# Kernel tuning notes

Measured on AMD Instinct MI355X. Metric: run time of the kernel, lower is better.

The kernel has to match this reference:

```python
import jax, jax.numpy as jnp
import numpy as np

# ---- grid / frustum config (from default grid_config & data_config) ----
DB = (1.0, 60.0, 1.0)                 # dbound
OGH, OGW, DS = 256, 704, 16           # input size, downsample
FH, FW = OGH // DS, OGW // DS         # 16, 44
DEPTH = int(round((DB[1] - DB[0]) / DB[2]))  # 59 depth bins
NX0, NX1, NZ = 128, 128, 1            # BEV grid
DX = np.array([0.8, 0.8, 20.0], np.float32)
BX = np.array([-51.2 + 0.4, -51.2 + 0.4, 0.0], np.float32)  # row0 + dx/2


def _frustum():
    # (D, FH, FW, 3): pixel (u, v, depth)
    ds = jnp.broadcast_to(jnp.arange(DB[0], DB[1], DB[2], dtype=jnp.float32).reshape(-1, 1, 1), (DEPTH, FH, FW))
    xs = jnp.broadcast_to(jnp.linspace(0.0, OGW - 1.0, FW, dtype=jnp.float32).reshape(1, 1, FW), (DEPTH, FH, FW))
    ys = jnp.broadcast_to(jnp.linspace(0.0, OGH - 1.0, FH, dtype=jnp.float32).reshape(1, FH, 1), (DEPTH, FH, FW))
    return jnp.stack([xs, ys, ds], axis=-1)


def _geometry(rots, trans, intrins, post_rots, post_trans, bda):
    # pixel frustum -> ego-frame 3D points; (B, N, D, FH, FW, 3)
    pts = _frustum() - post_trans[:, :, None, None, None, :]
    pts = jnp.einsum('bnij,bndhwj->bndhwi', jnp.linalg.inv(post_rots), pts)
    pts = jnp.concatenate([pts[..., :2] * pts[..., 2:3], pts[..., 2:3]], axis=-1)
    comb = jnp.einsum('bnij,bnjk->bnik', rots, jnp.linalg.inv(intrins))
    pts = jnp.einsum('bnij,bndhwj->bndhwi', comb, pts) + trans[:, :, None, None, None, :]
    pts = jnp.einsum('bij,bndhwj->bndhwi', bda, pts)
    return pts


def _voxel_pool(geom, vol):
    # geom: (B,N,D,FH,FW,3), vol: (B,N,D,FH,FW,C) -> BEV (B, C*NZ, NX0, NX1)
    B, C = vol.shape[0], vol.shape[-1]
    gidx = jnp.floor((geom - (BX - DX / 2.0)) / DX).astype(jnp.int32)
    kept = ((gidx[..., 0] >= 0) & (gidx[..., 0] < NX0)
            & (gidx[..., 1] >= 0) & (gidx[..., 1] < NX1)
            & (gidx[..., 2] >= 0) & (gidx[..., 2] < NZ))
    bidx = jnp.broadcast_to(jnp.arange(B, dtype=jnp.int32).reshape(B, 1, 1, 1, 1), gidx.shape[:-1])
    flat = ((bidx * NZ + gidx[..., 2]) * NX0 + gidx[..., 0]) * NX1 + gidx[..., 1]
    nvox = B * NZ * NX0 * NX1
    flat = jnp.where(kept, flat, nvox).reshape(-1)      # dump bucket for culled pts
    feats = vol.reshape(-1, C)
    bev = jax.ops.segment_sum(feats, flat, num_segments=nvox + 1)[:nvox]
    bev = bev.reshape(B, NZ, NX0, NX1, C)
    bev = jnp.moveaxis(bev, -1, 2).reshape(B, NZ * C, NX0, NX1)  # z-major channel cat
    return bev


def setup_inputs() -> dict:
    key = jax.random.key(0)
    B, N, CIN, CT = 4, 6, 512, 64
    k1, k2 = jax.random.split(key, 2)
    x = jax.random.normal(k1, (B, N, CIN, FH, FW), dtype=jnp.float32)
    weight = jax.random.normal(k2, (DEPTH + CT, CIN), dtype=jnp.float32) * 0.02
    bias = jnp.zeros((DEPTH + CT,), dtype=jnp.float32)
    # cam->ego rotation (cam z forward -> ego x, cam x right -> ego -y, cam y down -> ego -z)
    Rcam = jnp.asarray(np.array([[0., 0., 1.], [-1., 0., 0.], [0., -1., 0.]], np.float32))
    rots = jnp.tile(Rcam, (B, N, 1, 1))
    trans = jnp.zeros((B, N, 3), dtype=jnp.float32)
    K = jnp.asarray(np.array([[600., 0., 352.], [0., 600., 128.], [0., 0., 1.]], np.float32))
    intrins = jnp.tile(K, (B, N, 1, 1))
    post_rots = jnp.tile(jnp.eye(3, dtype=jnp.float32), (B, N, 1, 1))
    post_trans = jnp.zeros((B, N, 3), dtype=jnp.float32)
    bda = jnp.tile(jnp.eye(3, dtype=jnp.float32), (B, 1, 1))
    return dict(x=x, rots=rots, trans=trans, intrins=intrins, post_rots=post_rots,
                post_trans=post_trans, bda=bda, weight=weight, bias=bias)


def reference(x, rots, trans, intrins, post_rots, post_trans, bda, weight, bias):
    # 1x1 depth/context head (eval mode): (B,N,Cin,H,W) -> (B,N,D+C,H,W)
    out = jnp.einsum('bnchw,oc->bnohw', x, weight) + bias[None, None, :, None, None]
    depth = jax.nn.softmax(out[:, :, :DEPTH], axis=2)      # (B,N,D,H,W)
    feat = out[:, :, DEPTH:]                               # (B,N,C,H,W)
    # depth-context outer product -> frustum volume (B,N,D,H,W,C)
    vol = jnp.einsum('bndhw,bnchw->bndhwc', depth, feat)
    geom = _geometry(rots, trans, intrins, post_rots, post_trans, bda)
    bev = _voxel_pool(geom, vol)                           # (B, C*NZ, 128, 128)
    return bev, depth
```

## Files before the change

kernel.cpp:

```cpp
#include <hip/hip_runtime.h>
#include <math.h>

#define CIN   512
#define NOUT  123
#define DEPN  59
#define CT    64
#define B_    4
#define N_    6
#define FH    16
#define FW    44
#define HW    704
#define NPIX  (B_*N_*HW)
#define NX    128
#define BEV_ELEMS (B_*CT*NX*NX)
#define DEPTH_OFF BEV_ELEMS

#define WS_WB   1920
#define WS_PS   (WS_WB + 32768)
#define WS_FS   (WS_PS + NPIX*64)
#define WS_C    (WS_FS + NPIX*64)
#define WS_VOX  (WS_C + B_*FW*DEPN*64)
#define WS_MIXF (WS_VOX + B_*FW*DEPN)

typedef short bf16x8 __attribute__((ext_vector_type(8)));
typedef float f32x4  __attribute__((ext_vector_type(4)));

__device__ inline unsigned short f2bf(float f) {
    unsigned u = __float_as_uint(f);
    return (unsigned short)((u + 0x7fffu + ((u >> 16) & 1u)) >> 16);
}

__device__ inline void inv3d(const double* m, double* o) {
    #pragma clang fp contract(off)
    double c00 = m[4]*m[8] - m[5]*m[7];
    double c01 = m[5]*m[6] - m[3]*m[8];
    double c02 = m[3]*m[7] - m[4]*m[6];
    double det = m[0]*c00 + m[1]*c01 + m[2]*c02;
    o[0] = c00/det; o[1] = (m[2]*m[7]-m[1]*m[8])/det; o[2] = (m[1]*m[5]-m[2]*m[4])/det;
    o[3] = c01/det; o[4] = (m[0]*m[8]-m[2]*m[6])/det; o[5] = (m[2]*m[3]-m[0]*m[5])/det;
    o[6] = c02/det; o[7] = (m[1]*m[6]-m[0]*m[7])/det; o[8] = (m[0]*m[4]-m[1]*m[3])/det;
}
__device__ inline void mm3d(const double* a, const double* b, double* o) {
    #pragma clang fp contract(off)
    for (int i = 0; i < 3; ++i)
        for (int k = 0; k < 3; ++k)
            o[i*3+k] = (a[i*3+0]*b[0*3+k] + a[i*3+1]*b[1*3+k]) + a[i*3+2]*b[2*3+k];
}

#define K1A   4608
#define K1T   13824
__global__ __launch_bounds__(256, 2) void k1_gemm(const float* __restrict__ x,
                                                  const float* __restrict__ W,
                                                  const float* __restrict__ bias,
                                                  float* __restrict__ ws,
                                                  float* __restrict__ dout) {
    __shared__ __align__(16) unsigned short s16[2 * K1T];
    const int tid = threadIdx.x;
    const int wave = tid >> 6, lane = tid & 63;
    const int l15 = lane & 15, quad = lane >> 4;
    const int bn = blockIdx.y;
    const int pixbase = blockIdx.x * 64;
    const float* xg = x + (size_t)bn * CIN * HW + pixbase;
    const int cpack = tid >> 4;
    const int pix4 = (tid & 15) * 4;
    const int wo  = tid >> 3;
    const int wsub = tid & 7;

    f32x4 acc[8] = {};
    float4 xr0, xr1, xr2, xr3;
    float4 wf[8];
    const float4 zf4 = {0.f, 0.f, 0.f, 0.f};
    {
        const float* src = xg + (size_t)(4 * cpack) * HW + pix4;
        xr0 = *(const float4*)(src);
        xr1 = *(const float4*)(src + HW);
        xr2 = *(const float4*)(src + 2 * HW);
        xr3 = *(const float4*)(src + 3 * HW);
        #pragma unroll
        for (int i = 0; i < 4; ++i) {
            const int o = wo + 32 * i;
            if (o < NOUT) {
                const float* wp = W + (size_t)o * CIN + wsub * 8;
                wf[2 * i]     = *(const float4*)(wp);
                wf[2 * i + 1] = *(const float4*)(wp + 4);
            } else { wf[2 * i] = zf4; wf[2 * i + 1] = zf4; }
        }
    }
    #pragma unroll
    for (int it = 0; it < 8; ++it) {
        const int buf = it & 1;
        unsigned short* sa = s16 + buf * K1T;
        unsigned short* sb = sa + K1A;
        {
            const float* f0 = (const float*)&xr0; const float* f1 = (const float*)&xr1;
            const float* f2 = (const float*)&xr2; const float* f3 = (const float*)&xr3;
            #pragma unroll
            for (int i = 0; i < 4; ++i) {
                uint2 pk;
                pk.x = (unsigned)f2bf(f0[i]) | ((unsigned)f2bf(f1[i]) << 16);
                pk.y = (unsigned)f2bf(f2[i]) | ((unsigned)f2bf(f3[i]) << 16);
                *(uint2*)&sa[(pix4 + i) * 72 + 4 * cpack] = pk;
            }
            #pragma unroll
            for (int i = 0; i < 4; ++i) {
                const float* fw = (const float*)&wf[2 * i];
                uint4 pk;
                pk.x = (unsigned)f2bf(fw[0]) | ((unsigned)f2bf(fw[1]) << 16);
                pk.y = (unsigned)f2bf(fw[2]) | ((unsigned)f2bf(fw[3]) << 16);
                pk.z = (unsigned)f2bf(fw[4]) | ((unsigned)f2bf(fw[5]) << 16);
                pk.w = (unsigned)f2bf(fw[6]) | ((unsigned)f2bf(fw[7]) << 16);
                *(uint4*)&sb[(wo + 32 * i) * 72 + wsub * 8] = pk;
            }
        }
        if (it < 7) {
            const int ck = (it + 1) * 64;
            const float* src = xg + (size_t)(ck + 4 * cpack) * HW + pix4;
            xr0 = *(const float4*)(src);
            xr1 = *(const float4*)(src + HW);
            xr2 = *(const float4*)(src + 2 * HW);
            xr3 = *(const float4*)(src + 3 * HW);
            #pragma unroll
            for (int i = 0; i < 4; ++i) {
                const int o = wo + 32 * i;
                if (o < NOUT) {
                    const float* wp = W + (size_t)o * CIN + ck + wsub * 8;
                    wf[2 * i]     = *(const float4*)(wp);
                    wf[2 * i + 1] = *(const float4*)(wp + 4);
                } else { wf[2 * i] = zf4; wf[2 * i + 1] = zf4; }
            }
        }
        __syncthreads();
        #pragma unroll
        for (int ks = 0; ks < 64; ks += 32) {
            const bf16x8 a = *(const bf16x8*)&sa[(wave * 16 + l15) * 72 + ks + quad * 8];
            #pragma unroll
            for (int nt = 0; nt < 8; ++nt) {
                const bf16x8 b = *(const bf16x8*)&sb[(nt * 16 + l15) * 72 + ks + quad * 8];
                acc[nt] = __builtin_amdgcn_mfma_f32_16x16x32_bf16(a, b, acc[nt], 0, 0, 0);
            }
        }
    }
    float* sred = (float*)s16;
    const int b = bn / N_, n = bn - b * N_;
    {
        float bb[8];
        #pragma unroll
        for (int nt = 0; nt < 8; ++nt) {
            int o = nt * 16 + l15;
            bb[nt] = (o < NOUT) ? bias[o] : 0.0f;
        }
        float* ps = ws + WS_PS;
        float* fs = ws + WS_FS;
        #pragma unroll
        for (int reg = 0; reg < 4; ++reg) {
            int pixl = wave * 16 + quad * 4 + reg;
            int pix = pixbase + pixl;
            int h = pix / FW, w = pix - h * FW;
            size_t row = (size_t)(b * FW + w) * 96 + n * FH + h;
            float v[4]; float m = -INFINITY;
            #pragma unroll
            for (int nt = 0; nt < 4; ++nt) {
                v[nt] = acc[nt][reg] + bb[nt];
                if (nt * 16 + l15 < DEPN) m = fmaxf(m, v[nt]);
            }
            #pragma unroll
            for (int msk = 8; msk >= 1; msk >>= 1) m = fmaxf(m, __shfl_xor(m, msk, 64));
            float e[4], s = 0.0f;
            #pragma unroll
            for (int nt = 0; nt < 4; ++nt) {
                e[nt] = (nt * 16 + l15 < DEPN) ? expf(v[nt] - m) : 0.0f;
                s += e[nt];
            }
            #pragma unroll
            for (int msk = 8; msk >= 1; msk >>= 1) s += __shfl_xor(s, msk, 64);
            const float inv = 1.0f / s;
            #pragma unroll
            for (int nt = 0; nt < 4; ++nt) {
                int o = nt * 16 + l15;
                if (o < DEPN) {
                    float p = e[nt] * inv;
                    ps[row * 64 + o] = p;
                    sred[pixl * 65 + o] = p;
                } else fs[row * 64 + (o - DEPN)] = v[nt];
            }
            #pragma unroll
            for (int nt = 4; nt < 8; ++nt) {
                int o = nt * 16 + l15;
                if (o < NOUT) fs[row * 64 + (o - DEPN)] = acc[nt][reg] + bb[nt];
            }
        }
    }
    __syncthreads();
    for (int o = wave; o < DEPN; o += 4)
        dout[DEPTH_OFF + ((size_t)bn * DEPN + o) * HW + pixbase + lane] = sred[lane * 65 + o];
    {
        const int gbid = bn * 11 + blockIdx.x;
        float4 z = {0.f, 0.f, 0.f, 0.f};
        for (int i = gbid * 256 + tid; i < BEV_ELEMS / 4; i += 264 * 256)
            *(float4*)(dout + 4 * (size_t)i) = z;
        if (gbid == 0 && tid == 0) ((int*)(ws + WS_MIXF))[0] = 0;
    }
}

#define DQ2 16
__global__ __launch_bounds__(256) void k2b_geom(
        const float* __restrict__ rots,  const float* __restrict__ trans,
        const float* __restrict__ intr,  const float* __restrict__ prots,
        const float* __restrict__ ptrans,const float* __restrict__ bda,
        float* __restrict__ ws,          float* __restrict__ dout) {
    __shared__ float sF[96][64];
    __shared__ float sP[DQ2][100];
    __shared__ unsigned short sv16[DQ2 * 96];
    __shared__ __align__(16) double sG[96 * 9];
    __shared__ double sTd[N_][33];
    __shared__ int sflag[DQ2];
    const int tid = threadIdx.x;
    const int bw = blockIdx.x;
    const int b = bw / FW, w = bw - b * FW;
    const int dbase = blockIdx.y * DQ2;
    const int nd = min(DQ2, DEPN - dbase);

    {
        const float* fsrc = ws + WS_FS + (size_t)bw * (96 * 64);
        const float* psrc = ws + WS_PS + (size_t)bw * (96 * 64);
        for (int i = tid; i < 96 * 16; i += 256) {
            int j = i >> 4, c4 = (i & 15) * 4;
            *(float4*)&sF[j][c4] = *(const float4*)(fsrc + j * 64 + c4);
        }
        for (int i = tid; i < 96 * 4; i += 256) {
            int j = i >> 2, q = i & 3;
            const float4 p4 = *(const float4*)(psrc + j * 64 + dbase + 4 * q);
            sP[4 * q + 0][j] = p4.x; sP[4 * q + 1][j] = p4.y;
            sP[4 * q + 2][j] = p4.z; sP[4 * q + 3][j] = p4.w;
        }
    }
    if (tid < N_) {
        #pragma clang fp contract(off)
        int t = b * N_ + tid;
        double* X = sTd[tid];
        double PR[9], Kd[9], Rd[9], Bd[9];
        for (int i = 0; i < 9; ++i) PR[i] = (double)prots[t * 9 + i];
        for (int i = 0; i < 9; ++i) Kd[i] = (double)intr[t * 9 + i];
        for (int i = 0; i < 9; ++i) Rd[i] = (double)rots[t * 9 + i];
        for (int i = 0; i < 9; ++i) Bd[i] = (double)bda[b * 9 + i];
        double iPR[9]; inv3d(PR, iPR);
        for (int i = 0; i < 9; ++i) X[i] = iPR[i];
        for (int i = 0; i < 3; ++i) X[9 + i] = (double)ptrans[t * 3 + i];
        double iK[9];  inv3d(Kd, iK);
        double comb[9]; mm3d(Rd, iK, comb);
        for (int i = 0; i < 9; ++i) X[12 + i] = comb[i];
        for (int i = 0; i < 3; ++i) X[21 + i] = (double)trans[t * 3 + i];
        for (int i = 0; i < 9; ++i) X[24 + i] = Bd[i];
    }
    __syncthreads();
    if (tid < 96) {
        #pragma clang fp contract(off)
        int j = tid, n = j >> 4, h = j & 15;
        const double* T = sTd[n];
        const double xs = (w == 43) ? 703.0 : (double)w * (703.0 / 43.0);
        const double ys = (double)(h * 17);
        const double u0 = xs - T[9];
        const double u1 = ys - T[10];
        double pA[3], pB[3];
        #pragma unroll
        for (int k = 0; k < 3; ++k) {
            pA[k] = (T[3*k]*u0 + T[3*k+1]*u1) - T[3*k+2]*T[11];
            pB[k] = T[3*k+2];
        }
        double q0c[3] = { pA[0]*pA[2], pA[0]*pB[2] + pB[0]*pA[2], pB[0]*pB[2] };
        double q1c[3] = { pA[1]*pA[2], pA[1]*pB[2] + pB[1]*pA[2], pB[1]*pB[2] };
        double q2c[3] = { pA[2], pB[2], 0.0 };
        double rc[3][3], gc[3][3];
        #pragma unroll
        for (int r = 0; r < 3; ++r)
            #pragma unroll
            for (int k = 0; k < 3; ++k)
                rc[r][k] = ((T[12+3*r]*q0c[k] + T[13+3*r]*q1c[k]) + T[14+3*r]*q2c[k])
                           + ((k == 0) ? T[21+r] : 0.0);
        #pragma unroll
        for (int g = 0; g < 3; ++g)
            #pragma unroll
            for (int k = 0; k < 3; ++k)
                gc[g][k] = (T[24+3*g]*rc[0][k] + T[25+3*g]*rc[1][k]) + T[26+3*g]*rc[2][k];
        #pragma unroll
        for (int q = 0; q < 9; ++q) sG[j * 9 + q] = gc[q / 3][q % 3];
    }
    __syncthreads();

    {
        const double BXY = (double)(-51.2000007629394531f);
        for (int idx = tid; idx < nd * 96; idx += 256) {
            int dl = idx / 96, j = idx - dl * 96;
            const double* G = &sG[j * 9];
            const double dsv = (double)(dbase + dl + 1);
            const double g0 = (G[2] * dsv + G[1]) * dsv + G[0];
            const double g1 = (G[5] * dsv + G[4]) * dsv + G[3];
            const double g2 = (G[8] * dsv + G[7]) * dsv + G[6];
            const double fx = floor((g0 - BXY) * 1.25);
            const double fy = floor((g1 - BXY) * 1.25);
            const bool keep = (fx >= 0.0) & (fx < 128.0) & (fy >= 0.0) & (fy < 128.0) &
                              (g2 >= -10.0) & (g2 < 10.0);
            sv16[idx] = keep ? (unsigned short)((int)fx * NX + (int)fy)
                             : (unsigned short)0xFFFF;
        }
    }
    __syncthreads();

    {
        const int dl = tid >> 4, s = tid & 15;
        int u = -1, mix = 0;
        const int base = dl * 96 + s * 6;
        #pragma unroll
        for (int t = 0; t < 6; ++t) {
            int v = sv16[base + t];
            if (v != 0xFFFF) { if (u < 0) u = v; else if (v != u) mix = 1; }
        }
        #pragma unroll
        for (int msk = 1; msk < 16; msk <<= 1) {
            int uo = __shfl_xor(u, msk, 64);
            int mo = __shfl_xor(mix, msk, 64);
            mix = mix | mo | ((u >= 0 && uo >= 0 && uo != u) ? 1 : 0);
            u = (u < 0) ? uo : u;
        }
        if (s == 0 && dl < nd) sflag[dl] = mix ? -2 : u;
    }
    for (int idx = tid; idx < nd * 96; idx += 256) {
        if (sv16[idx] == 0xFFFF) {
            int dl = idx / 96, j = idx - dl * 96;
            sP[dl][j] = 0.0f;
        }
    }
    __syncthreads();

    const int dl = tid >> 4, ci = tid & 15;
    if (dl < nd) {
        const int flag = sflag[dl];
        if (ci == 0)
            ((int*)(ws + WS_VOX))[bw * DEPN + dbase + dl] = (flag >= 0) ? flag : -1;
        if (flag >= 0) {
            float ax = 0.f, ay = 0.f, az = 0.f, aw = 0.f;
            for (int jj = 0; jj < 96; jj += 4) {
                const float4 pv = *(const float4*)&sP[dl][jj];
                const float4 f0 = *(const float4*)&sF[jj + 0][4 * ci];
                const float4 f1 = *(const float4*)&sF[jj + 1][4 * ci];
                const float4 f2 = *(const float4*)&sF[jj + 2][4 * ci];
                const float4 f3 = *(const float4*)&sF[jj + 3][4 * ci];
                ax = fmaf(pv.x, f0.x, ax); ay = fmaf(pv.x, f0.y, ay);
                az = fmaf(pv.x, f0.z, az); aw = fmaf(pv.x, f0.w, aw);
                ax = fmaf(pv.y, f1.x, ax); ay = fmaf(pv.y, f1.y, ay);
                az = fmaf(pv.y, f1.z, az); aw = fmaf(pv.y, f1.w, aw);
                ax = fmaf(pv.z, f2.x, ax); ay = fmaf(pv.z, f2.y, ay);
                az = fmaf(pv.z, f2.z, az); aw = fmaf(pv.z, f2.w, aw);
                ax = fmaf(pv.w, f3.x, ax); ay = fmaf(pv.w, f3.y, ay);
                az = fmaf(pv.w, f3.z, az); aw = fmaf(pv.w, f3.w, aw);
            }
            float4 st = { ax, ay, az, aw };
            *(float4*)&ws[WS_C + ((size_t)(bw * DEPN + dbase + dl)) * 64 + 4 * ci] = st;
        }
    }
    for (int d2 = 0; d2 < nd; ++d2) {
        if (sflag[d2] == -2) {
            if (tid == 0) atomicOr((int*)(ws + WS_MIXF), 1);
            int c = tid & 63, g = tid >> 6;
            for (int jj = 0; jj < 24; ++jj) {
                int j = g * 24 + jj;
                int v = sv16[d2 * 96 + j];
                if (v != 0xFFFF)
                    atomicAdd(dout + (((size_t)(b * CT + c)) << 14) + v,
                              sP[d2][j] * sF[j][c]);
            }
        }
    }
}

#define CHUNK 128
__global__ __launch_bounds__(256) void k2c_scatter(const float* __restrict__ ws,
                                                   float* __restrict__ dout) {
    __shared__ float acc[64][CHUNK + 4];
    __shared__ int   sVox[FW * DEPN];
    __shared__ short sMatch[FW * DEPN];
    __shared__ int   nMatch;
    const int tid = threadIdx.x;
    const int base = blockIdx.x * CHUNK;
    const int b = blockIdx.y;
    for (int i = tid; i < 64 * (CHUNK + 4); i += 256) (&acc[0][0])[i] = 0.0f;
    if (tid == 0) nMatch = 0;
    const int* vsrc = (const int*)(ws + WS_VOX) + b * (FW * DEPN);
    for (int i = tid; i < FW * DEPN; i += 256) sVox[i] = vsrc[i];
    __syncthreads();
    for (int i = tid; i < FW * DEPN; i += 256) {
        int v = sVox[i];
        if ((unsigned)(v - base) < CHUNK) {
            int m = atomicAdd(&nMatch, 1);
            sMatch[m] = (short)i;
        }
    }
    __syncthreads();
    const int c = tid & 63, quarter = tid >> 6;
    const int nm = nMatch;
    for (int m = quarter; m < nm; m += 4) {
        int e = sMatch[m];
        int lv = sVox[e] - base;
        float val = ws[WS_C + ((size_t)b * (FW * DEPN) + e) * 64 + c];
        atomicAdd(&acc[c][lv], val);
    }
    __syncthreads();
    const int mixed = ((const int*)(ws + WS_MIXF))[0];
    const int wave = tid >> 6, lane = tid & 63;
    float* outb = dout + (((size_t)(b * CT)) << 14) + base;
    if (!mixed) {
        for (int r = wave; r < 64; r += 4) {
            float2 v = { acc[r][lane * 2], acc[r][lane * 2 + 1] };
            *(float2*)(outb + ((size_t)r << 14) + lane * 2) = v;
        }
    } else {
        for (int r = wave; r < 64; r += 4) {
            float2* dst = (float2*)(outb + ((size_t)r << 14) + lane * 2);
            float2 v = *dst;
            v.x += acc[r][lane * 2];
            v.y += acc[r][lane * 2 + 1];
            *dst = v;
        }
    }
}

extern "C" void kernel_launch(void* const* d_in, const int* in_sizes, int n_in,
                              void* d_out, int out_size, void* d_ws, size_t ws_size,
                              hipStream_t stream) {
    const float* x      = (const float*)d_in[0];
    const float* rots   = (const float*)d_in[1];
    const float* trans  = (const float*)d_in[2];
    const float* intr   = (const float*)d_in[3];
    const float* prots  = (const float*)d_in[4];
    const float* ptrans = (const float*)d_in[5];
    const float* bda    = (const float*)d_in[6];
    const float* W      = (const float*)d_in[7];
    const float* bias   = (const float*)d_in[8];
    float* out = (float*)d_out;
    float* ws  = (float*)d_ws;

    k1_gemm<<<dim3(HW / 64, B_ * N_), 256, 0, stream>>>(x, W, bias, ws, out);
    k2b_geom<<<dim3(B_ * FW, 4), 256, 0, stream>>>(rots, trans, intr, prots, ptrans,
                                                   bda, ws, out);
    k2c_scatter<<<dim3(NX * NX / CHUNK, B_), 256, 0, stream>>>(ws, out);
}
```

Baseline: 137.5 us.

## Split GEMM output channels across blocks and replace BEV zero-fill with overflow buffer

The 1x1 conv GEMM now splits its 128 output columns across two blocks per pixel tile, which doubles the grid and halves per-block accumulators and LDS. The first half handles softmax and depth, the second writes context features. The full BEV zero-fill in k1 and the global atomicAdd into the output for mixed-voxel rows are removed. Those contributions are instead appended to a workspace overflow list, which k2c_scatter folds into its shared accumulators before writing each chunk. This makes the final store a plain overwrite, at the cost of x being loaded twice and every scatter block scanning the overflow list.

```diff
diff --git a/kernel.cpp b/kernel.cpp
--- a/kernel.cpp
+++ b/kernel.cpp
@@ -20,7 +20,10 @@
 #define WS_FS   (WS_PS + NPIX*64)
 #define WS_C    (WS_FS + NPIX*64)
 #define WS_VOX  (WS_C + B_*FW*DEPN*64)
-#define WS_MIXF (WS_VOX + B_*FW*DEPN)
+#define WS_OVN  (WS_VOX + B_*FW*DEPN)
+#define WS_OVK  (WS_OVN + 8)
+#define WS_OVD  (WS_OVK + 16384)
+#define OVCAP   16384
 
 typedef short bf16x8 __attribute__((ext_vector_type(8)));
 typedef float f32x4  __attribute__((ext_vector_type(4)));
@@ -48,27 +51,30 @@
 }
 
 #define K1A   4608
-#define K1T   13824
-__global__ __launch_bounds__(256, 2) void k1_gemm(const float* __restrict__ x,
-                                                  const float* __restrict__ W,
-                                                  const float* __restrict__ bias,
-                                                  float* __restrict__ ws,
-                                                  float* __restrict__ dout) {
+#define K1T   9216
+__global__ __launch_bounds__(256) void k1_gemm(const float* __restrict__ x,
+                                               const float* __restrict__ W,
+                                               const float* __restrict__ bias,
+                                               float* __restrict__ ws,
+                                               float* __restrict__ dout) {
     __shared__ __align__(16) unsigned short s16[2 * K1T];
     const int tid = threadIdx.x;
     const int wave = tid >> 6, lane = tid & 63;
     const int l15 = lane & 15, quad = lane >> 4;
     const int bn = blockIdx.y;
-    const int pixbase = blockIdx.x * 64;
+    const int px = blockIdx.x >> 1;
+    const int oh = blockIdx.x & 1;
+    const int pixbase = px * 64;
+    const int o0 = oh * 64;
     const float* xg = x + (size_t)bn * CIN * HW + pixbase;
     const int cpack = tid >> 4;
     const int pix4 = (tid & 15) * 4;
     const int wo  = tid >> 3;
     const int wsub = tid & 7;
 
-    f32x4 acc[8] = {};
+    f32x4 acc[4] = {};
     float4 xr0, xr1, xr2, xr3;
-    float4 wf[8];
+    float4 wf[4];
     const float4 zf4 = {0.f, 0.f, 0.f, 0.f};
     {
         const float* src = xg + (size_t)(4 * cpack) * HW + pix4;
@@ -77,8 +83,8 @@
         xr2 = *(const float4*)(src + 2 * HW);
         xr3 = *(const float4*)(src + 3 * HW);
         #pragma unroll
-        for (int i = 0; i < 4; ++i) {
-            const int o = wo + 32 * i;
+        for (int i = 0; i < 2; ++i) {
+            const int o = o0 + wo + 32 * i;
             if (o < NOUT) {
                 const float* wp = W + (size_t)o * CIN + wsub * 8;
                 wf[2 * i]     = *(const float4*)(wp);
@@ -102,7 +108,7 @@
                 *(uint2*)&sa[(pix4 + i) * 72 + 4 * cpack] = pk;
             }
             #pragma unroll
-            for (int i = 0; i < 4; ++i) {
+            for (int i = 0; i < 2; ++i) {
                 const float* fw = (const float*)&wf[2 * i];
                 uint4 pk;
                 pk.x = (unsigned)f2bf(fw[0]) | ((unsigned)f2bf(fw[1]) << 16);
@@ -120,8 +126,8 @@
             xr2 = *(const float4*)(src + 2 * HW);
             xr3 = *(const float4*)(src + 3 * HW);
             #pragma unroll
-            for (int i = 0; i < 4; ++i) {
-                const int o = wo + 32 * i;
+            for (int i = 0; i < 2; ++i) {
+                const int o = o0 + wo + 32 * i;
                 if (o < NOUT) {
                     const float* wp = W + (size_t)o * CIN + ck + wsub * 8;
                     wf[2 * i]     = *(const float4*)(wp);
@@ -134,7 +140,7 @@
         for (int ks = 0; ks < 64; ks += 32) {
             const bf16x8 a = *(const bf16x8*)&sa[(wave * 16 + l15) * 72 + ks + quad * 8];
             #pragma unroll
-            for (int nt = 0; nt < 8; ++nt) {
+            for (int nt = 0; nt < 4; ++nt) {
                 const bf16x8 b = *(const bf16x8*)&sb[(nt * 16 + l15) * 72 + ks + quad * 8];
                 acc[nt] = __builtin_amdgcn_mfma_f32_16x16x32_bf16(a, b, acc[nt], 0, 0, 0);
             }
@@ -143,10 +149,10 @@
     float* sred = (float*)s16;
     const int b = bn / N_, n = bn - b * N_;
     {
-        float bb[8];
-        #pragma unroll
-        for (int nt = 0; nt < 8; ++nt) {
-            int o = nt * 16 + l15;
+        float bb[4];
+        #pragma unroll
+        for (int nt = 0; nt < 4; ++nt) {
+            int o = o0 + nt * 16 + l15;
             bb[nt] = (o < NOUT) ? bias[o] : 0.0f;
         }
         float* ps = ws + WS_PS;
@@ -157,49 +163,50 @@
             int pix = pixbase + pixl;
             int h = pix / FW, w = pix - h * FW;
             size_t row = (size_t)(b * FW + w) * 96 + n * FH + h;
-            float v[4]; float m = -INFINITY;
-            #pragma unroll
-            for (int nt = 0; nt < 4; ++nt) {
-                v[nt] = acc[nt][reg] + bb[nt];
-                if (nt * 16 + l15 < DEPN) m = fmaxf(m, v[nt]);
-            }
-            #pragma unroll
-            for (int msk = 8; msk >= 1; msk >>= 1) m = fmaxf(m, __shfl_xor(m, msk, 64));
-            float e[4], s = 0.0f;
-            #pragma unroll
-            for (int nt = 0; nt < 4; ++nt) {
-                e[nt] = (nt * 16 + l15 < DEPN) ? expf(v[nt] - m) : 0.0f;
-                s += e[nt];
-            }
-            #pragma unroll
-            for (int msk = 8; msk >= 1; msk >>= 1) s += __shfl_xor(s, msk, 64);
-            const float inv = 1.0f / s;
-            #pragma unroll
-            for (int nt = 0; nt < 4; ++nt) {
-                int o = nt * 16 + l15;
-                if (o < DEPN) {
-                    float p = e[nt] * inv;
-                    ps[row * 64 + o] = p;
-                    sred[pixl * 65 + o] = p;
-                } else fs[row * 64 + (o - DEPN)] = v[nt];
-            }
-            #pragma unroll
-            for (int nt = 4; nt < 8; ++nt) {
-                int o = nt * 16 + l15;
-                if (o < NOUT) fs[row * 64 + (o - DEPN)] = acc[nt][reg] + bb[nt];
-            }
-        }
-    }
-    __syncthreads();
-    for (int o = wave; o < DEPN; o += 4)
-        dout[DEPTH_OFF + ((size_t)bn * DEPN + o) * HW + pixbase + lane] = sred[lane * 65 + o];
-    {
-        const int gbid = bn * 11 + blockIdx.x;
-        float4 z = {0.f, 0.f, 0.f, 0.f};
-        for (int i = gbid * 256 + tid; i < BEV_ELEMS / 4; i += 264 * 256)
-            *(float4*)(dout + 4 * (size_t)i) = z;
-        if (gbid == 0 && tid == 0) ((int*)(ws + WS_MIXF))[0] = 0;
-    }
+            if (oh == 0) {
+                float v[4]; float m = -INFINITY;
+                #pragma unroll
+                for (int nt = 0; nt < 4; ++nt) {
+                    v[nt] = acc[nt][reg] + bb[nt];
+                    if (nt * 16 + l15 < DEPN) m = fmaxf(m, v[nt]);
+                }
+                #pragma unroll
+                for (int msk = 8; msk >= 1; msk >>= 1) m = fmaxf(m, __shfl_xor(m, msk, 64));
+                float e[4], s = 0.0f;
+                #pragma unroll
+                for (int nt = 0; nt < 4; ++nt) {
+                    e[nt] = (nt * 16 + l15 < DEPN) ? expf(v[nt] - m) : 0.0f;
+                    s += e[nt];
+                }
+                #pragma unroll
+                for (int msk = 8; msk >= 1; msk >>= 1) s += __shfl_xor(s, msk, 64);
+                const float inv = 1.0f / s;
+                #pragma unroll
+                for (int nt = 0; nt < 4; ++nt) {
+                    int o = nt * 16 + l15;
+                    if (o < DEPN) {
+                        float p = e[nt] * inv;
+                        ps[row * 64 + o] = p;
+                        sred[pixl * 65 + o] = p;
+                    } else fs[row * 64 + (o - DEPN)] = v[nt];
+                }
+            } else {
+                #pragma unroll
+                for (int nt = 0; nt < 4; ++nt) {
+                    int o = o0 + nt * 16 + l15;
+                    if (o < NOUT) fs[row * 64 + (o - DEPN)] = acc[nt][reg] + bb[nt];
+                }
+            }
+        }
+    }
+    __syncthreads();
+    if (oh == 0) {
+        for (int o = wave; o < DEPN; o += 4)
+            dout[DEPTH_OFF + ((size_t)bn * DEPN + o) * HW + pixbase + lane] =
+                sred[lane * 65 + o];
+    }
+    if (blockIdx.x == 0 && blockIdx.y == 0 && tid == 0)
+        ((int*)(ws + WS_OVN))[0] = 0;
 }
 
 #define DQ2 16
@@ -207,7 +214,7 @@
         const float* __restrict__ rots,  const float* __restrict__ trans,
         const float* __restrict__ intr,  const float* __restrict__ prots,
         const float* __restrict__ ptrans,const float* __restrict__ bda,
-        float* __restrict__ ws,          float* __restrict__ dout) {
+        float* __restrict__ ws) {
     __shared__ float sF[96][64];
     __shared__ float sP[DQ2][100];
     __shared__ unsigned short sv16[DQ2 * 96];
@@ -360,14 +367,19 @@
     }
     for (int d2 = 0; d2 < nd; ++d2) {
         if (sflag[d2] == -2) {
-            if (tid == 0) atomicOr((int*)(ws + WS_MIXF), 1);
             int c = tid & 63, g = tid >> 6;
             for (int jj = 0; jj < 24; ++jj) {
                 int j = g * 24 + jj;
                 int v = sv16[d2 * 96 + j];
-                if (v != 0xFFFF)
-                    atomicAdd(dout + (((size_t)(b * CT + c)) << 14) + v,
-                              sP[d2][j] * sF[j][c]);
+                if (v != 0xFFFF) {
+                    int slot = 0;
+                    if (c == 0) slot = atomicAdd((int*)(ws + WS_OVN), 1);
+                    slot = __shfl(slot, 0, 64);
+                    if (slot < OVCAP) {
+                        if (c == 0) ((int*)(ws + WS_OVK))[slot] = (b << 14) | v;
+                        ws[WS_OVD + (size_t)slot * 64 + c] = sP[d2][j] * sF[j][c];
+                    }
+                }
             }
         }
     }
@@ -404,23 +416,22 @@
         float val = ws[WS_C + ((size_t)b * (FW * DEPN) + e) * 64 + c];
         atomicAdd(&acc[c][lv], val);
     }
-    __syncthreads();
-    const int mixed = ((const int*)(ws + WS_MIXF))[0];
+    {
+        int nov = ((const int*)(ws + WS_OVN))[0];
+        if (nov > OVCAP) nov = OVCAP;
+        for (int m = quarter; m < nov; m += 4) {
+            int key = ((const int*)(ws + WS_OVK))[m];
+            int lv = (key & 16383) - base;
+            if ((key >> 14) == b && (unsigned)lv < CHUNK)
+                atomicAdd(&acc[c][lv], ws[WS_OVD + (size_t)m * 64 + c]);
+        }
+    }
+    __syncthreads();
     const int wave = tid >> 6, lane = tid & 63;
     float* outb = dout + (((size_t)(b * CT)) << 14) + base;
-    if (!mixed) {
-        for (int r = wave; r < 64; r += 4) {
-            float2 v = { acc[r][lane * 2], acc[r][lane * 2 + 1] };
-            *(float2*)(outb + ((size_t)r << 14) + lane * 2) = v;
-        }
-    } else {
-        for (int r = wave; r < 64; r += 4) {
-            float2* dst = (float2*)(outb + ((size_t)r << 14) + lane * 2);
-            float2 v = *dst;
-            v.x += acc[r][lane * 2];
-            v.y += acc[r][lane * 2 + 1];
-            *dst = v;
-        }
+    for (int r = wave; r < 64; r += 4) {
+        float2 v = { acc[r][lane * 2], acc[r][lane * 2 + 1] };
+        *(float2*)(outb + ((size_t)r << 14) + lane * 2) = v;
     }
 }
 
@@ -439,8 +450,8 @@
     float* out = (float*)d_out;
     float* ws  = (float*)d_ws;
 
-    k1_gemm<<<dim3(HW / 64, B_ * N_), 256, 0, stream>>>(x, W, bias, ws, out);
+    k1_gemm<<<dim3((HW / 64) * 2, B_ * N_), 256, 0, stream>>>(x, W, bias, ws, out);
     k2b_geom<<<dim3(B_ * FW, 4), 256, 0, stream>>>(rots, trans, intr, prots, ptrans,
-                                                   bda, ws, out);
+                                                   bda, ws);
     k2c_scatter<<<dim3(NX * NX / CHUNK, B_), 256, 0, stream>>>(ws, out);
 }
```

After: 137.0 us. No clear change (-0.3%).
